# Performance work log

Measured on AMD Instinct MI355X. Metric: run time of the kernel, lower is better.

## Reference

```python
import jax, jax.numpy as jnp
import numpy as np

NUM_NODES = 100000
NUM_EDGES = 1600000
DIM = 64
NUM_LAYERS = 3


def setup_inputs() -> dict:
    key = jax.random.key(0)
    k1, k2 = jax.random.split(key)
    x = jax.random.normal(k1, (NUM_NODES, DIM), dtype=jnp.float32)
    adj_t = jax.random.randint(k2, (2, NUM_EDGES), 0, NUM_NODES, dtype=jnp.int64)
    return {"x": x, "adj_t": adj_t}


def reference(x, adj_t):
    n = x.shape[0]
    # undirected -> add reversed edges (adj_t_is_undirected=True path)
    edge_index = jnp.concatenate([adj_t, adj_t[::-1]], axis=1)  # [2, 2E]
    row, col = edge_index[0], edge_index[1]
    edge_weight = jnp.ones((row.shape[0],), dtype=x.dtype)
    # gcn_norm: D^-0.5 A D^-0.5 (degree computed by scatter over col)
    deg = jax.ops.segment_sum(edge_weight, col, num_segments=n)
    deg_inv_sqrt = jnp.where(deg > 0, jax.lax.rsqrt(deg), 0.0).astype(x.dtype)
    w = deg_inv_sqrt[row] * edge_weight * deg_inv_sqrt[col]  # [2E]
    outs = [x]
    for _ in range(NUM_LAYERS):
        # gather -> scale -> scatter_add (SpMM)
        msgs = w[:, None] * x[row]                     # [2E, D]
        x = jax.ops.segment_sum(msgs, col, num_segments=n)  # [N, D]
        outs.append(x)
    return jnp.mean(jnp.stack(outs), axis=0)
```

## Files before the change

kernel.cpp:

```cpp
#include <hip/hip_runtime.h>

#define DIM 64
#define SCAN_B 256
#define BKT_SHIFT 7
#define BKT_G 128
#define NBLK 256
#define HIST_B 1024

__device__ inline float blo(unsigned p) { return __uint_as_float(p << 16); }
__device__ inline float bhi(unsigned p) { return __uint_as_float(p & 0xffff0000u); }
__device__ inline unsigned bpack(float x, float y) {
    unsigned ux = __float_as_uint(x);
    unsigned uy = __float_as_uint(y);
    ux += 0x7fffu + ((ux >> 16) & 1u);
    uy += 0x7fffu + ((uy >> 16) & 1u);
    return (ux >> 16) | (uy & 0xffff0000u);
}

__global__ __launch_bounds__(HIST_B)
void hist_kernel(const int* __restrict__ adj, int E,
                 int* __restrict__ hist, int NB) {
    extern __shared__ int lh[];
    for (int g = threadIdx.x; g < NB; g += blockDim.x) lh[g] = 0;
    __syncthreads();
    for (int e = blockIdx.x * blockDim.x + threadIdx.x; e < E;
         e += NBLK * blockDim.x) {
        int a = adj[e];
        int b = adj[E + e];
        atomicAdd(&lh[a >> BKT_SHIFT], 1);
        atomicAdd(&lh[b >> BKT_SHIFT], 1);
    }
    __syncthreads();
    for (int g = threadIdx.x; g < NB; g += blockDim.x)
        hist[g * NBLK + blockIdx.x] = lh[g];
}

__global__ void scan_block_kernel(const int* __restrict__ src, int n,
                                  int* __restrict__ dst,
                                  int* __restrict__ blocksums) {
    __shared__ int tmp[SCAN_B];
    int i = blockIdx.x * SCAN_B + threadIdx.x;
    int v = (i < n) ? src[i] : 0;
    tmp[threadIdx.x] = v;
    __syncthreads();
    for (int off = 1; off < SCAN_B; off <<= 1) {
        int t = (threadIdx.x >= off) ? tmp[threadIdx.x - off] : 0;
        __syncthreads();
        tmp[threadIdx.x] += t;
        __syncthreads();
    }
    if (i < n) dst[i] = tmp[threadIdx.x] - v;
    if (threadIdx.x == SCAN_B - 1) blocksums[blockIdx.x] = tmp[SCAN_B - 1];
}

__global__ void scan_sums_kernel(int* __restrict__ blocksums, int nb) {
    __shared__ int tmp[1024];
    int v = (threadIdx.x < nb) ? blocksums[threadIdx.x] : 0;
    tmp[threadIdx.x] = v;
    __syncthreads();
    for (int off = 1; off < 1024; off <<= 1) {
        int t = (threadIdx.x >= off) ? tmp[threadIdx.x - off] : 0;
        __syncthreads();
        tmp[threadIdx.x] += t;
        __syncthreads();
    }
    if (threadIdx.x < nb) blocksums[threadIdx.x] = tmp[threadIdx.x] - v;
}

__global__ void scan_add_kernel(int* __restrict__ dst,
                                const int* __restrict__ blocksums,
                                int n, int total) {
    int i = blockIdx.x * blockDim.x + threadIdx.x;
    if (i < n) dst[i] += blocksums[i / SCAN_B];
    if (i == n) dst[n] = total;
}

__global__ __launch_bounds__(HIST_B)
void place_kernel(const int* __restrict__ adj, int E,
                  const int* __restrict__ hist_s,
                  unsigned* __restrict__ pairs, int NB) {
    extern __shared__ int cur[];
    for (int g = threadIdx.x; g < NB; g += blockDim.x)
        cur[g] = hist_s[g * NBLK + blockIdx.x];
    __syncthreads();
    for (int e = blockIdx.x * blockDim.x + threadIdx.x; e < E;
         e += NBLK * blockDim.x) {
        int a = adj[e];
        int b = adj[E + e];
        int pb = atomicAdd(&cur[b >> BKT_SHIFT], 1);
        pairs[pb] = ((unsigned)(b & (BKT_G - 1)) << 17) | (unsigned)a;
        int pa = atomicAdd(&cur[a >> BKT_SHIFT], 1);
        pairs[pa] = ((unsigned)(a & (BKT_G - 1)) << 17) | (unsigned)b;
    }
}

__global__ void pass2_build_kernel(const unsigned* __restrict__ pairs,
                                   const int* __restrict__ hist_s,
                                   const float4* __restrict__ x,
                                   int* __restrict__ csr_src,
                                   int* __restrict__ row_ptr,
                                   int* __restrict__ deg,
                                   float* __restrict__ dinv,
                                   uint4* __restrict__ xs0,
                                   int N, int total_adj) {
    __shared__ int cnt[BKT_G];
    __shared__ int pre[BKT_G];
    __shared__ int cur[BKT_G];
    __shared__ float dv[BKT_G];
    int g = blockIdx.x;
    int base = g << BKT_SHIFT;
    int off = hist_s[(size_t)g * NBLK];
    int offn = (g + 1 < gridDim.x) ? hist_s[(size_t)(g + 1) * NBLK] : total_adj;
    int m = offn - off;
    if (threadIdx.x < BKT_G) cnt[threadIdx.x] = 0;
    __syncthreads();
    for (int i = threadIdx.x; i < m; i += blockDim.x)
        atomicAdd(&cnt[pairs[off + i] >> 17], 1);
    __syncthreads();
    if (threadIdx.x < BKT_G) pre[threadIdx.x] = cnt[threadIdx.x];
    __syncthreads();
    for (int o = 1; o < BKT_G; o <<= 1) {
        int t = 0;
        if (threadIdx.x < BKT_G && threadIdx.x >= o) t = pre[threadIdx.x - o];
        __syncthreads();
        if (threadIdx.x < BKT_G) pre[threadIdx.x] += t;
        __syncthreads();
    }
    if (threadIdx.x < BKT_G) {
        int v = base + threadIdx.x;
        if (v < N) {
            int c = cnt[threadIdx.x];
            int start = off + pre[threadIdx.x] - c;
            float di = (c > 0) ? rsqrtf((float)c) : 0.0f;
            row_ptr[v] = start;
            deg[v] = c;
            dinv[v] = di;
            dv[threadIdx.x] = di;
            cur[threadIdx.x] = start;
        }
    }
    if (g == gridDim.x - 1 && threadIdx.x == 0) row_ptr[N] = total_adj;
    __syncthreads();
    for (int i = threadIdx.x; i < m; i += blockDim.x) {
        unsigned p = pairs[off + i];
        int dl  = (int)(p >> 17);
        int src = (int)(p & 0x1ffffu);
        int pos = atomicAdd(&cur[dl], 1);
        csr_src[pos] = src;
    }
    for (int w = threadIdx.x; w < BKT_G * 8; w += blockDim.x) {
        int vl = w >> 3, sub = w & 7;
        int v = base + vl;
        if (v < N) {
            float di = dv[vl];
            float4 xa = x[(size_t)v * 16 + sub * 2];
            float4 xb = x[(size_t)v * 16 + sub * 2 + 1];
            uint4 o;
            o.x = bpack(di * xa.x, di * xa.y);
            o.y = bpack(di * xa.z, di * xa.w);
            o.z = bpack(di * xb.x, di * xb.y);
            o.w = bpack(di * xb.z, di * xb.w);
            xs0[(size_t)v * 8 + sub] = o;
        }
    }
}

__global__ void spmm_bf16_kernel(const int* __restrict__ row_ptr,
                                 const int* __restrict__ csr_src,
                                 const float* __restrict__ dinv,
                                 const uint4* __restrict__ xs_in,
                                 uint4* __restrict__ xs_out, int N) {
    int t = blockIdx.x * blockDim.x + threadIdx.x;
    int v = t >> 5;
    if (v >= N) return;
    int half = threadIdx.x & 31;
    int nb = half >> 3, sub = half & 7;
    int beg = row_ptr[v];
    int end = row_ptr[v + 1];
    float a0 = 0, a1 = 0, a2 = 0, a3 = 0, a4 = 0, a5 = 0, a6 = 0, a7 = 0;
    int i0 = beg + nb, i1 = beg + nb + 4;
    int s0 = (i0 < end) ? csr_src[i0] : -1;
    int s1 = (i1 < end) ? csr_src[i1] : -1;
    for (int j = beg; j < end; j += 8) {
        int ni0 = j + 8 + nb, ni1 = j + 12 + nb;
        int t0 = (ni0 < end) ? csr_src[ni0] : -1;
        int t1 = (ni1 < end) ? csr_src[ni1] : -1;
        uint4 p0 = xs_in[(size_t)(s0 >= 0 ? s0 : 0) * 8 + sub];
        uint4 p1 = xs_in[(size_t)(s1 >= 0 ? s1 : 0) * 8 + sub];
        float m0 = (s0 >= 0) ? 1.0f : 0.0f;
        float m1 = (s1 >= 0) ? 1.0f : 0.0f;
        a0 += m0 * blo(p0.x); a1 += m0 * bhi(p0.x);
        a2 += m0 * blo(p0.y); a3 += m0 * bhi(p0.y);
        a4 += m0 * blo(p0.z); a5 += m0 * bhi(p0.z);
        a6 += m0 * blo(p0.w); a7 += m0 * bhi(p0.w);
        a0 += m1 * blo(p1.x); a1 += m1 * bhi(p1.x);
        a2 += m1 * blo(p1.y); a3 += m1 * bhi(p1.y);
        a4 += m1 * blo(p1.z); a5 += m1 * bhi(p1.z);
        a6 += m1 * blo(p1.w); a7 += m1 * bhi(p1.w);
        s0 = t0; s1 = t1;
    }
    a0 += __shfl_xor(a0, 8);  a0 += __shfl_xor(a0, 16);
    a1 += __shfl_xor(a1, 8);  a1 += __shfl_xor(a1, 16);
    a2 += __shfl_xor(a2, 8);  a2 += __shfl_xor(a2, 16);
    a3 += __shfl_xor(a3, 8);  a3 += __shfl_xor(a3, 16);
    a4 += __shfl_xor(a4, 8);  a4 += __shfl_xor(a4, 16);
    a5 += __shfl_xor(a5, 8);  a5 += __shfl_xor(a5, 16);
    a6 += __shfl_xor(a6, 8);  a6 += __shfl_xor(a6, 16);
    a7 += __shfl_xor(a7, 8);  a7 += __shfl_xor(a7, 16);
    if (nb == 0) {
        float di = dinv[v];
        float d2 = di * di;
        uint4 o;
        o.x = bpack(d2 * a0, d2 * a1);
        o.y = bpack(d2 * a2, d2 * a3);
        o.z = bpack(d2 * a4, d2 * a5);
        o.w = bpack(d2 * a6, d2 * a7);
        xs_out[(size_t)v * 8 + sub] = o;
    }
}

__global__ void final_kernel(const float4* __restrict__ x,
                             const int* __restrict__ deg,
                             const uint4* __restrict__ xs1,
                             const uint4* __restrict__ xs2,
                             const uint4* __restrict__ xs3,
                             float4* __restrict__ out, int N) {
    int t = blockIdx.x * blockDim.x + threadIdx.x;
    int v = t >> 3, sub = t & 7;
    if (v >= N) return;
    size_t idx = (size_t)v * 8 + sub;
    uint4 p1 = xs1[idx], p2 = xs2[idx], p3 = xs3[idx];
    float rs = sqrtf((float)deg[v]);
    float s0 = blo(p1.x) + blo(p2.x) + blo(p3.x);
    float s1 = bhi(p1.x) + bhi(p2.x) + bhi(p3.x);
    float s2 = blo(p1.y) + blo(p2.y) + blo(p3.y);
    float s3 = bhi(p1.y) + bhi(p2.y) + bhi(p3.y);
    float s4 = blo(p1.z) + blo(p2.z) + blo(p3.z);
    float s5 = bhi(p1.z) + bhi(p2.z) + bhi(p3.z);
    float s6 = blo(p1.w) + blo(p2.w) + blo(p3.w);
    float s7 = bhi(p1.w) + bhi(p2.w) + bhi(p3.w);
    float4 xa = x[(size_t)v * 16 + sub * 2];
    float4 xb = x[(size_t)v * 16 + sub * 2 + 1];
    float4 oa, ob;
    oa.x = 0.25f * (xa.x + rs * s0);
    oa.y = 0.25f * (xa.y + rs * s1);
    oa.z = 0.25f * (xa.z + rs * s2);
    oa.w = 0.25f * (xa.w + rs * s3);
    ob.x = 0.25f * (xb.x + rs * s4);
    ob.y = 0.25f * (xb.y + rs * s5);
    ob.z = 0.25f * (xb.z + rs * s6);
    ob.w = 0.25f * (xb.w + rs * s7);
    out[(size_t)v * 16 + sub * 2]     = oa;
    out[(size_t)v * 16 + sub * 2 + 1] = ob;
}

extern "C" void kernel_launch(void* const* d_in, const int* in_sizes, int n_in,
                              void* d_out, int out_size, void* d_ws, size_t ws_size,
                              hipStream_t stream) {
    const float* x = (const float*)d_in[0];
    const int* adj = (const int*)d_in[1];
    float* out     = (float*)d_out;

    const int total_adj = in_sizes[1];
    const int E = total_adj / 2;
    const int N = in_sizes[0] / DIM;
    const int NB = (N + BKT_G - 1) / BKT_G;
    const int nhist = NB * NBLK;

    size_t BUF = (size_t)total_adj * 4;
    size_t xsb = (size_t)N * 32 * 4;
    if (xsb > BUF) BUF = xsb;
    BUF = (BUF + 255) & ~(size_t)255;

    char* ws = (char*)d_ws;
    int*      deg     = (int*)(ws);
    float*    dinv    = (float*)(ws + (size_t)512 * 1024);
    int*      row_ptr = (int*)(ws + (size_t)1024 * 1024);
    int*      bsums   = (int*)(ws + (size_t)1536 * 1024);
    int*      hist    = (int*)(ws + (size_t)1600 * 1024);
    int*      hist_s  = (int*)(ws + (size_t)2432 * 1024);
    char*     big     = ws + (size_t)3264 * 1024;
    int*      csr_src = (int*)(big);
    unsigned* pairs   = (unsigned*)(big + BUF);
    uint4*    xs0     = (uint4*)(big + BUF);
    uint4*    xs1     = (uint4*)(big + 2 * BUF);
    uint4*    xs2     = (uint4*)(big + 3 * BUF);
    uint4*    xs3     = (uint4*)(big + 4 * BUF);
    uint4*    xs0_s   = (uint4*)(big + 5 * BUF);

    const int B = 256;

    hist_kernel<<<NBLK, HIST_B, NB * sizeof(int), stream>>>(adj, E, hist, NB);

    const int nscan2 = (nhist + SCAN_B - 1) / SCAN_B;
    scan_block_kernel<<<nscan2, SCAN_B, 0, stream>>>(hist, nhist, hist_s, bsums);
    scan_sums_kernel<<<1, 1024, 0, stream>>>(bsums, nscan2);
    scan_add_kernel<<<(nhist + 1 + B - 1) / B, B, 0, stream>>>(hist_s, bsums, nhist, total_adj);

    place_kernel<<<NBLK, HIST_B, NB * sizeof(int), stream>>>(adj, E, hist_s, pairs, NB);

    pass2_build_kernel<<<NB, B, 0, stream>>>(pairs, hist_s, (const float4*)x,
                                             csr_src, row_ptr, deg, dinv,
                                             xs0_s, N, total_adj);

    const int nblocks32 = (int)(((long long)N * 32 + B - 1) / B);
    spmm_bf16_kernel<<<nblocks32, B, 0, stream>>>(row_ptr, csr_src, dinv, xs0_s, xs1, N);
    spmm_bf16_kernel<<<nblocks32, B, 0, stream>>>(row_ptr, csr_src, dinv, xs1, xs2, N);
    spmm_bf16_kernel<<<nblocks32, B, 0, stream>>>(row_ptr, csr_src, dinv, xs2, xs3, N);

    const int nblocks8 = (int)(((long long)N * 8 + B - 1) / B);
    final_kernel<<<nblocks8, B, 0, stream>>>((const float4*)x, deg, xs1, xs2, xs3,
                                             (float4*)out, N);
}
```

Measured before the change: 302.2 us.

## Fuse final averaging into last SpMM and unroll neighbor gather by four

The third SpMM layer now writes the final output directly, reading x, xs1 and xs2 in its epilogue. This removes the separate final kernel and the bf16 round trip through xs3. The accumulation loop also changes: each lane now handles four contiguous neighbors per 16-edge chunk, followed by a remainder loop. That replaces the masked two-neighbor loop and gives more loads in flight per iteration. The cost is higher register pressure, and the contiguous per-lane index layout changes the access pattern for csr_src.

```diff
diff --git a/kernel.cpp b/kernel.cpp
--- a/kernel.cpp
+++ b/kernel.cpp
@@ -165,6 +165,60 @@
     }
 }
 
+#define SPMM_ACCUM_BODY                                                        \
+    int half = threadIdx.x & 31;                                               \
+    int nb = half >> 3, sub = half & 7;                                        \
+    int beg = row_ptr[v];                                                      \
+    int end = row_ptr[v + 1];                                                  \
+    int full = (end - beg) >> 4;                                               \
+    float a0 = 0, a1 = 0, a2 = 0, a3 = 0, a4 = 0, a5 = 0, a6 = 0, a7 = 0;      \
+    int j = beg;                                                               \
+    int s0 = 0, s1 = 0, s2 = 0, s3 = 0;                                        \
+    if (full > 0) {                                                            \
+        int b = j + 4 * nb;                                                    \
+        s0 = csr_src[b];     s1 = csr_src[b + 1];                              \
+        s2 = csr_src[b + 2]; s3 = csr_src[b + 3];                              \
+    }                                                                          \
+    for (int it = 0; it < full; ++it) {                                        \
+        int jn = j + 16;                                                       \
+        int t0 = 0, t1 = 0, t2 = 0, t3 = 0;                                    \
+        if (it + 1 < full) {                                                   \
+            int b = jn + 4 * nb;                                               \
+            t0 = csr_src[b];     t1 = csr_src[b + 1];                          \
+            t2 = csr_src[b + 2]; t3 = csr_src[b + 3];                          \
+        }                                                                      \
+        uint4 p0 = xs_in[(size_t)s0 * 8 + sub];                                \
+        uint4 p1 = xs_in[(size_t)s1 * 8 + sub];                                \
+        uint4 p2 = xs_in[(size_t)s2 * 8 + sub];                                \
+        uint4 p3 = xs_in[(size_t)s3 * 8 + sub];                                \
+        a0 += (blo(p0.x) + blo(p1.x)) + (blo(p2.x) + blo(p3.x));               \
+        a1 += (bhi(p0.x) + bhi(p1.x)) + (bhi(p2.x) + bhi(p3.x));               \
+        a2 += (blo(p0.y) + blo(p1.y)) + (blo(p2.y) + blo(p3.y));               \
+        a3 += (bhi(p0.y) + bhi(p1.y)) + (bhi(p2.y) + bhi(p3.y));               \
+        a4 += (blo(p0.z) + blo(p1.z)) + (blo(p2.z) + blo(p3.z));               \
+        a5 += (bhi(p0.z) + bhi(p1.z)) + (bhi(p2.z) + bhi(p3.z));               \
+        a6 += (blo(p0.w) + blo(p1.w)) + (blo(p2.w) + blo(p3.w));               \
+        a7 += (bhi(p0.w) + bhi(p1.w)) + (bhi(p2.w) + bhi(p3.w));               \
+        s0 = t0; s1 = t1; s2 = t2; s3 = t3;                                    \
+        j = jn;                                                                \
+    }                                                                          \
+    for (int idx = j + nb; idx < end; idx += 4) {                              \
+        int s = csr_src[idx];                                                  \
+        uint4 p = xs_in[(size_t)s * 8 + sub];                                  \
+        a0 += blo(p.x); a1 += bhi(p.x);                                        \
+        a2 += blo(p.y); a3 += bhi(p.y);                                        \
+        a4 += blo(p.z); a5 += bhi(p.z);                                        \
+        a6 += blo(p.w); a7 += bhi(p.w);                                        \
+    }                                                                          \
+    a0 += __shfl_xor(a0, 8);  a0 += __shfl_xor(a0, 16);                        \
+    a1 += __shfl_xor(a1, 8);  a1 += __shfl_xor(a1, 16);                        \
+    a2 += __shfl_xor(a2, 8);  a2 += __shfl_xor(a2, 16);                        \
+    a3 += __shfl_xor(a3, 8);  a3 += __shfl_xor(a3, 16);                        \
+    a4 += __shfl_xor(a4, 8);  a4 += __shfl_xor(a4, 16);                        \
+    a5 += __shfl_xor(a5, 8);  a5 += __shfl_xor(a5, 16);                        \
+    a6 += __shfl_xor(a6, 8);  a6 += __shfl_xor(a6, 16);                        \
+    a7 += __shfl_xor(a7, 8);  a7 += __shfl_xor(a7, 16);
+
 __global__ void spmm_bf16_kernel(const int* __restrict__ row_ptr,
                                  const int* __restrict__ csr_src,
                                  const float* __restrict__ dinv,
@@ -173,40 +227,7 @@
     int t = blockIdx.x * blockDim.x + threadIdx.x;
     int v = t >> 5;
     if (v >= N) return;
-    int half = threadIdx.x & 31;
-    int nb = half >> 3, sub = half & 7;
-    int beg = row_ptr[v];
-    int end = row_ptr[v + 1];
-    float a0 = 0, a1 = 0, a2 = 0, a3 = 0, a4 = 0, a5 = 0, a6 = 0, a7 = 0;
-    int i0 = beg + nb, i1 = beg + nb + 4;
-    int s0 = (i0 < end) ? csr_src[i0] : -1;
-    int s1 = (i1 < end) ? csr_src[i1] : -1;
-    for (int j = beg; j < end; j += 8) {
-        int ni0 = j + 8 + nb, ni1 = j + 12 + nb;
-        int t0 = (ni0 < end) ? csr_src[ni0] : -1;
-        int t1 = (ni1 < end) ? csr_src[ni1] : -1;
-        uint4 p0 = xs_in[(size_t)(s0 >= 0 ? s0 : 0) * 8 + sub];
-        uint4 p1 = xs_in[(size_t)(s1 >= 0 ? s1 : 0) * 8 + sub];
-        float m0 = (s0 >= 0) ? 1.0f : 0.0f;
-        float m1 = (s1 >= 0) ? 1.0f : 0.0f;
-        a0 += m0 * blo(p0.x); a1 += m0 * bhi(p0.x);
-        a2 += m0 * blo(p0.y); a3 += m0 * bhi(p0.y);
-        a4 += m0 * blo(p0.z); a5 += m0 * bhi(p0.z);
-        a6 += m0 * blo(p0.w); a7 += m0 * bhi(p0.w);
-        a0 += m1 * blo(p1.x); a1 += m1 * bhi(p1.x);
-        a2 += m1 * blo(p1.y); a3 += m1 * bhi(p1.y);
-        a4 += m1 * blo(p1.z); a5 += m1 * bhi(p1.z);
-        a6 += m1 * blo(p1.w); a7 += m1 * bhi(p1.w);
-        s0 = t0; s1 = t1;
-    }
-    a0 += __shfl_xor(a0, 8);  a0 += __shfl_xor(a0, 16);
-    a1 += __shfl_xor(a1, 8);  a1 += __shfl_xor(a1, 16);
-    a2 += __shfl_xor(a2, 8);  a2 += __shfl_xor(a2, 16);
-    a3 += __shfl_xor(a3, 8);  a3 += __shfl_xor(a3, 16);
-    a4 += __shfl_xor(a4, 8);  a4 += __shfl_xor(a4, 16);
-    a5 += __shfl_xor(a5, 8);  a5 += __shfl_xor(a5, 16);
-    a6 += __shfl_xor(a6, 8);  a6 += __shfl_xor(a6, 16);
-    a7 += __shfl_xor(a7, 8);  a7 += __shfl_xor(a7, 16);
+    SPMM_ACCUM_BODY
     if (nb == 0) {
         float di = dinv[v];
         float d2 = di * di;
@@ -219,39 +240,38 @@
     }
 }
 
-__global__ void final_kernel(const float4* __restrict__ x,
-                             const int* __restrict__ deg,
-                             const uint4* __restrict__ xs1,
-                             const uint4* __restrict__ xs2,
-                             const uint4* __restrict__ xs3,
-                             float4* __restrict__ out, int N) {
+__global__ void spmm_last_kernel(const int* __restrict__ row_ptr,
+                                 const int* __restrict__ csr_src,
+                                 const float* __restrict__ dinv,
+                                 const int* __restrict__ deg,
+                                 const uint4* __restrict__ xs_in,
+                                 const uint4* __restrict__ xs1,
+                                 const float4* __restrict__ x,
+                                 float4* __restrict__ out, int N) {
     int t = blockIdx.x * blockDim.x + threadIdx.x;
-    int v = t >> 3, sub = t & 7;
+    int v = t >> 5;
     if (v >= N) return;
-    size_t idx = (size_t)v * 8 + sub;
-    uint4 p1 = xs1[idx], p2 = xs2[idx], p3 = xs3[idx];
-    float rs = sqrtf((float)deg[v]);
-    float s0 = blo(p1.x) + blo(p2.x) + blo(p3.x);
-    float s1 = bhi(p1.x) + bhi(p2.x) + bhi(p3.x);
-    float s2 = blo(p1.y) + blo(p2.y) + blo(p3.y);
-    float s3 = bhi(p1.y) + bhi(p2.y) + bhi(p3.y);
-    float s4 = blo(p1.z) + blo(p2.z) + blo(p3.z);
-    float s5 = bhi(p1.z) + bhi(p2.z) + bhi(p3.z);
-    float s6 = blo(p1.w) + blo(p2.w) + blo(p3.w);
-    float s7 = bhi(p1.w) + bhi(p2.w) + bhi(p3.w);
-    float4 xa = x[(size_t)v * 16 + sub * 2];
-    float4 xb = x[(size_t)v * 16 + sub * 2 + 1];
-    float4 oa, ob;
-    oa.x = 0.25f * (xa.x + rs * s0);
-    oa.y = 0.25f * (xa.y + rs * s1);
-    oa.z = 0.25f * (xa.z + rs * s2);
-    oa.w = 0.25f * (xa.w + rs * s3);
-    ob.x = 0.25f * (xb.x + rs * s4);
-    ob.y = 0.25f * (xb.y + rs * s5);
-    ob.z = 0.25f * (xb.z + rs * s6);
-    ob.w = 0.25f * (xb.w + rs * s7);
-    out[(size_t)v * 16 + sub * 2]     = oa;
-    out[(size_t)v * 16 + sub * 2 + 1] = ob;
+    SPMM_ACCUM_BODY
+    if (nb == 0) {
+        float di = dinv[v];
+        float rs = sqrtf((float)deg[v]);
+        size_t idx = (size_t)v * 8 + sub;
+        uint4 q1 = xs1[idx];
+        uint4 q2 = xs_in[idx];
+        float4 xa = x[(size_t)v * 16 + sub * 2];
+        float4 xb = x[(size_t)v * 16 + sub * 2 + 1];
+        float4 oa, ob;
+        oa.x = 0.25f * (xa.x + rs * (blo(q1.x) + blo(q2.x)) + di * a0);
+        oa.y = 0.25f * (xa.y + rs * (bhi(q1.x) + bhi(q2.x)) + di * a1);
+        oa.z = 0.25f * (xa.z + rs * (blo(q1.y) + blo(q2.y)) + di * a2);
+        oa.w = 0.25f * (xa.w + rs * (bhi(q1.y) + bhi(q2.y)) + di * a3);
+        ob.x = 0.25f * (xb.x + rs * (blo(q1.z) + blo(q2.z)) + di * a4);
+        ob.y = 0.25f * (xb.y + rs * (bhi(q1.z) + bhi(q2.z)) + di * a5);
+        ob.z = 0.25f * (xb.z + rs * (blo(q1.w) + blo(q2.w)) + di * a6);
+        ob.w = 0.25f * (xb.w + rs * (bhi(q1.w) + bhi(q2.w)) + di * a7);
+        out[(size_t)v * 16 + sub * 2]     = oa;
+        out[(size_t)v * 16 + sub * 2 + 1] = ob;
+    }
 }
 
 extern "C" void kernel_launch(void* const* d_in, const int* in_sizes, int n_in,
@@ -282,11 +302,9 @@
     char*     big     = ws + (size_t)3264 * 1024;
     int*      csr_src = (int*)(big);
     unsigned* pairs   = (unsigned*)(big + BUF);
-    uint4*    xs0     = (uint4*)(big + BUF);
-    uint4*    xs1     = (uint4*)(big + 2 * BUF);
-    uint4*    xs2     = (uint4*)(big + 3 * BUF);
-    uint4*    xs3     = (uint4*)(big + 4 * BUF);
-    uint4*    xs0_s   = (uint4*)(big + 5 * BUF);
+    uint4*    xs0     = (uint4*)(big + 2 * BUF);
+    uint4*    xs1     = (uint4*)(big + 3 * BUF);
+    uint4*    xs2     = (uint4*)(big + 4 * BUF);
 
     const int B = 256;
 
@@ -301,14 +319,12 @@
 
     pass2_build_kernel<<<NB, B, 0, stream>>>(pairs, hist_s, (const float4*)x,
                                              csr_src, row_ptr, deg, dinv,
-                                             xs0_s, N, total_adj);
+                                             xs0, N, total_adj);
 
     const int nblocks32 = (int)(((long long)N * 32 + B - 1) / B);
-    spmm_bf16_kernel<<<nblocks32, B, 0, stream>>>(row_ptr, csr_src, dinv, xs0_s, xs1, N);
+    spmm_bf16_kernel<<<nblocks32, B, 0, stream>>>(row_ptr, csr_src, dinv, xs0, xs1, N);
     spmm_bf16_kernel<<<nblocks32, B, 0, stream>>>(row_ptr, csr_src, dinv, xs1, xs2, N);
-    spmm_bf16_kernel<<<nblocks32, B, 0, stream>>>(row_ptr, csr_src, dinv, xs2, xs3, N);
-
-    const int nblocks8 = (int)(((long long)N * 8 + B - 1) / B);
-    final_kernel<<<nblocks8, B, 0, stream>>>((const float4*)x, deg, xs1, xs2, xs3,
-                                             (float4*)out, N);
-}
+    spmm_last_kernel<<<nblocks32, B, 0, stream>>>(row_ptr, csr_src, dinv, deg,
+                                                  xs2, xs1, (const float4*)x,
+                                                  (float4*)out, N);
+}
```

After: 300.9 us. About the same (-0.4%).
